# Kernel optimization log

Hardware: AMD Instinct MI355X
Metric: run time of the kernel (lower is better)

The kernel has to match this reference:

```python
import jax, jax.numpy as jnp
import numpy as np

N = 100000   # nodes
E = 1600000  # edges
DIN, DH, DOUT = 64, 128, 128


def setup_inputs() -> dict:
    key = jax.random.key(0)
    ks = jax.random.split(key, 12)
    x = jax.random.normal(ks[0], (N, DIN), dtype=jnp.float32)
    edge_index = jax.random.randint(ks[1], (2, E), 0, N, dtype=jnp.int32)
    s = 1.0 / np.sqrt(DIN)
    W1 = jax.random.uniform(ks[2], (DIN, DH), jnp.float32, -s, s)
    b1 = jnp.zeros((DH,), jnp.float32)
    g1 = jnp.ones((DH,), jnp.float32)
    bt1 = jnp.zeros((DH,), jnp.float32)
    s2 = 1.0 / np.sqrt(DH)
    W2 = jax.random.uniform(ks[3], (DH, DOUT), jnp.float32, -s2, s2)
    b2 = jnp.zeros((DOUT,), jnp.float32)
    g2 = jnp.ones((DOUT,), jnp.float32)
    bt2 = jnp.zeros((DOUT,), jnp.float32)
    return {"x": x, "edge_index": edge_index, "W1": W1, "b1": b1, "g1": g1,
            "bt1": bt1, "W2": W2, "b2": b2, "g2": g2, "bt2": bt2}


def _layer_norm(h, g, b, eps=1e-5):
    mu = h.mean(-1, keepdims=True)
    var = h.var(-1, keepdims=True)
    return (h - mu) * jax.lax.rsqrt(var + eps) * g + b


def reference(x, edge_index, W1, b1, g1, bt1, W2, b2, g2, bt2):
    # GCN normalization with self-loops (shared graph structure for both layers)
    src, dst = edge_index[0], edge_index[1]
    loops = jnp.arange(N, dtype=src.dtype)
    src = jnp.concatenate([src, loops])
    dst = jnp.concatenate([dst, loops])
    deg = jax.ops.segment_sum(jnp.ones_like(src, jnp.float32), dst, num_segments=N)
    dinv = jnp.where(deg > 0, jax.lax.rsqrt(deg), 0.0)
    norm = dinv[src] * dinv[dst]  # [E+N]

    def gcn(h, W, b):
        hw = h @ W                         # linear first (PyG GCNConv)
        msg = hw[src] * norm[:, None]      # gather + edge scale
        return jax.ops.segment_sum(msg, dst, num_segments=N) + b

    h = jax.nn.relu(_layer_norm(gcn(x, W1, b1), g1, bt1))
    # dropout is identity at inference
    h = jax.nn.relu(_layer_norm(gcn(h, W2, b2), g2, bt2))
    return h
```

## Files before the change

kernel.cpp:

```cpp
#include <hip/hip_runtime.h>

#define NN 100000
#define NE 1600000
#define NBKT 196
#define CAP 12288
#define EPB 8192
#define ABLK ((NE + EPB - 1) / EPB)
typedef unsigned short u16;
typedef unsigned int u32;

typedef __attribute__((ext_vector_type(8))) short short8v;
typedef __attribute__((ext_vector_type(4))) float f32x4;

__device__ __forceinline__ u32 f2bf(float f) {
    u32 u = __float_as_uint(f);
    return (u + 0x7fffu + ((u >> 16) & 1u)) >> 16;
}
__device__ __forceinline__ u32 pack2(float a, float b) {
    return f2bf(a) | (f2bf(b) << 16);
}
__device__ __forceinline__ void accum8(float* a, uint4 u, float w) {
    a[0] += __uint_as_float(u.x << 16) * w;
    a[1] += __uint_as_float(u.x & 0xffff0000u) * w;
    a[2] += __uint_as_float(u.y << 16) * w;
    a[3] += __uint_as_float(u.y & 0xffff0000u) * w;
    a[4] += __uint_as_float(u.z << 16) * w;
    a[5] += __uint_as_float(u.z & 0xffff0000u) * w;
    a[6] += __uint_as_float(u.w << 16) * w;
    a[7] += __uint_as_float(u.w & 0xffff0000u) * w;
}

__global__ __launch_bounds__(256) void kA_bin(const int* __restrict__ src,
                                              const int* __restrict__ dst,
                                              int* __restrict__ gcnt,
                                              u32* __restrict__ binned) {
    __shared__ int bc[NBKT];
    __shared__ int cbase[NBKT];
    const int tid = threadIdx.x;
    for (int i = tid; i < NBKT; i += 256) bc[i] = 0;
    __syncthreads();
    const int e0 = blockIdx.x * EPB;
#pragma unroll
    for (int i = 0; i < EPB / 256; ++i) {
        const int e = e0 + i * 256 + tid;
        if (e < NE) atomicAdd(&bc[dst[e] >> 9], 1);
    }
    __syncthreads();
    for (int i = tid; i < NBKT; i += 256)
        cbase[i] = bc[i] ? atomicAdd(&gcnt[i], bc[i]) : 0;
    __syncthreads();
    for (int i = tid; i < NBKT; i += 256) bc[i] = 0;
    __syncthreads();
#pragma unroll
    for (int i = 0; i < EPB / 256; ++i) {
        const int e = e0 + i * 256 + tid;
        if (e < NE) {
            const int d = dst[e];
            const int bkt = d >> 9;
            const int p = atomicAdd(&bc[bkt], 1);
            binned[bkt * CAP + cbase[bkt] + p] = ((u32)src[e] << 9) | (u32)(d & 511);
        }
    }
}

__global__ __launch_bounds__(256) void kB_fill(const u32* __restrict__ binned,
                                               const int* __restrict__ gcnt,
                                               int2* __restrict__ off2,
                                               float* __restrict__ dinv,
                                               int* __restrict__ csr,
                                               const float* __restrict__ x,
                                               u16* __restrict__ xb) {
    __shared__ int lcnt[512];
    __shared__ int lpos[512];
    __shared__ float sdinv[512];
    __shared__ int ws[4];
    const int b = blockIdx.x;
    const int tid = threadIdx.x;
    const int cnt = gcnt[b];
    const int base0 = b * CAP;
    const int node0 = b << 9;
    lcnt[tid] = 0;
    lcnt[tid + 256] = 0;
    __syncthreads();
    for (int e = tid; e < cnt; e += 256)
        atomicAdd(&lcnt[binned[base0 + e] & 511], 1);
    __syncthreads();
    const int c0 = lcnt[tid * 2], c1 = lcnt[tid * 2 + 1];
    const int s = c0 + c1;
    const int lane = tid & 63, w = tid >> 6;
    int incl = s;
#pragma unroll
    for (int o = 1; o < 64; o <<= 1) {
        const int u = __shfl_up(incl, o);
        if (lane >= o) incl += u;
    }
    if (lane == 63) ws[w] = incl;
    __syncthreads();
    int base = incl - s;
    for (int i = 0; i < w; ++i) base += ws[i];
    lpos[tid * 2] = base;
    lpos[tid * 2 + 1] = base + c0;
    const float d0 = rsqrtf(1.0f + (float)c0);
    const float d1 = rsqrtf(1.0f + (float)c1);
    sdinv[tid * 2] = d0;
    sdinv[tid * 2 + 1] = d1;
    const int n0 = node0 + tid * 2;
    if (n0 < NN) {
        off2[n0] = make_int2(base0 + base, base0 + base + c0);
        dinv[n0] = d0;
    }
    if (n0 + 1 < NN) {
        off2[n0 + 1] = make_int2(base0 + base + c0, base0 + base + c0 + c1);
        dinv[n0 + 1] = d1;
    }
    __syncthreads();
    for (int e = tid; e < cnt; e += 256) {
        const u32 u = binned[base0 + e];
        const int p = atomicAdd(&lpos[u & 511], 1);
        csr[base0 + p] = (int)(u >> 9);
    }
    const int nmax = min(512, NN - node0);
    for (int gi = tid; gi < nmax * 8; gi += 256) {
        const int nl = gi >> 3, ch = gi & 7;
        const float dr = sdinv[nl];
        const size_t xo = (size_t)(node0 + nl) * 64 + ch * 8;
        const float4 v0 = *(const float4*)&x[xo];
        const float4 v1 = *(const float4*)&x[xo + 4];
        uint4 o;
        o.x = pack2(v0.x * dr, v0.y * dr); o.y = pack2(v0.z * dr, v0.w * dr);
        o.z = pack2(v1.x * dr, v1.y * dr); o.w = pack2(v1.z * dr, v1.w * dr);
        *(uint4*)&xb[xo] = o;
    }
}

__global__ __launch_bounds__(256) void k_prep(const float* __restrict__ W1,
                                              const float* __restrict__ W2,
                                              u16* __restrict__ WT1,
                                              u16* __restrict__ WT2,
                                              int* __restrict__ gcnt) {
    const int i = blockIdx.x * 256 + threadIdx.x;
    if (i < 8192) {
        const int k = i >> 7, c = i & 127;
        WT1[c * 64 + k] = (u16)f2bf(W1[i]);
    } else if (i < 24576) {
        const int i2 = i - 8192;
        const int k = i2 >> 7, c = i2 & 127;
        WT2[c * 128 + k] = (u16)f2bf(W2[i2]);
    } else if (i < 24576 + NBKT) {
        gcnt[i - 24576] = 0;
    }
}

template<int K, bool FP32OUT, bool PRESCALE>
__global__ __launch_bounds__(256) void k_fused(const u16* __restrict__ A,
                                               const int2* __restrict__ off2,
                                               const int* __restrict__ csr,
                                               const float* __restrict__ dinv,
                                               const u16* __restrict__ WT,
                                               const float* __restrict__ bias,
                                               const float* __restrict__ g,
                                               const float* __restrict__ bt,
                                               void* __restrict__ outp) {
    constexpr int RB = K * 2;
    constexpr int SUBS = 512 / K;
    constexpr int LSH = (K == 64) ? 7 : 8;
    __shared__ u16 As[32 * K];
    __shared__ float s1s[4][32];
    __shared__ float s2s[4][32];
    __shared__ int claim;
    const int tid = threadIdx.x;
    const int wv = tid >> 6, lane = tid & 63;
    const int sub = lane / (64 / SUBS);
    const int l = lane & (64 / SUBS - 1);
    const char* Ab = (const char*)A + ((u32)l << 4);
    const int nodeBase = blockIdx.x * 32;

    if (tid == 0) claim = 0;
    __syncthreads();

    int i;
    if (lane == 0) i = atomicAdd(&claim, 1);
    i = __builtin_amdgcn_readfirstlane(i);
    while (i < 32) {
        const int node = nodeBase + i;
        const float di = dinv[node];
        float a[8] = {};
        {
            const uint4 u = *(const uint4*)(Ab + ((u32)node << LSH));
            accum8(a, u, (sub == 0) ? 1.0f : 0.0f);
        }
        const int2 oe = off2[node];
        int base = oe.x;
        const int e1 = oe.y;
        u32 iA = 0, iB = 0, iC = 0;
        float vA = 0.f, vB = 0.f, vC = 0.f;
        if (base < e1) {
            const int eA = base + sub, eB = eA + SUBS, eC = eA + 2 * SUBS;
            iA = (u32)csr[min(eA, e1 - 1)];
            iB = (u32)csr[min(eB, e1 - 1)];
            iC = (u32)csr[min(eC, e1 - 1)];
            vA = (eA < e1) ? 1.f : 0.f;
            vB = (eB < e1) ? 1.f : 0.f;
            vC = (eC < e1) ? 1.f : 0.f;
        }
        while (base < e1) {
            const uint4 uA = *(const uint4*)(Ab + (iA << LSH));
            const uint4 uB = *(const uint4*)(Ab + (iB << LSH));
            const uint4 uC = *(const uint4*)(Ab + (iC << LSH));
            const float wA = vA, wB = vB, wC = vC;
            base += 3 * SUBS;
            if (base < e1) {
                const int eA = base + sub, eB = eA + SUBS, eC = eA + 2 * SUBS;
                iA = (u32)csr[min(eA, e1 - 1)];
                iB = (u32)csr[min(eB, e1 - 1)];
                iC = (u32)csr[min(eC, e1 - 1)];
                vA = (eA < e1) ? 1.f : 0.f;
                vB = (eB < e1) ? 1.f : 0.f;
                vC = (eC < e1) ? 1.f : 0.f;
            }
            accum8(a, uA, wA);
            accum8(a, uB, wB);
            accum8(a, uC, wC);
        }
#pragma unroll
        for (int t = 0; t < 8; ++t)
#pragma unroll
            for (int o = 64 / SUBS; o < 64; o <<= 1)
                a[t] += __shfl_xor(a[t], o);
        if (sub == 0) {
            uint4 o;
            o.x = pack2(a[0] * di, a[1] * di); o.y = pack2(a[2] * di, a[3] * di);
            o.z = pack2(a[4] * di, a[5] * di); o.w = pack2(a[6] * di, a[7] * di);
            *(uint4*)((char*)As + i * RB + (((u32)l << 4) ^ ((u32)(i & 7) << 4))) = o;
        }
        if (lane == 0) i = atomicAdd(&claim, 1);
        i = __builtin_amdgcn_readfirstlane(i);
    }
    __syncthreads();

    const int lr = lane & 15, kg = lane >> 4;
    short8v af[2][K / 32];
#pragma unroll
    for (int rt = 0; rt < 2; ++rt)
#pragma unroll
        for (int kk = 0; kk < K / 32; ++kk)
            af[rt][kk] = *(const short8v*)((const char*)As + (rt * 16 + lr) * RB +
                                           ((u32)(kk * 64 + kg * 16) ^ ((u32)(lr & 7) << 4)));
    f32x4 acc[2][2];
    float bv[2], gv[2], tv[2];
#pragma unroll
    for (int nt = 0; nt < 2; ++nt) {
        acc[0][nt] = (f32x4){0.f, 0.f, 0.f, 0.f};
        acc[1][nt] = (f32x4){0.f, 0.f, 0.f, 0.f};
        const int col = wv * 32 + nt * 16 + lr;
        short8v bf[K / 32];
#pragma unroll
        for (int kk = 0; kk < K / 32; ++kk)
            bf[kk] = *(const short8v*)&WT[col * K + kk * 32 + kg * 8];
#pragma unroll
        for (int rt = 0; rt < 2; ++rt)
#pragma unroll
            for (int kk = 0; kk < K / 32; ++kk)
                acc[rt][nt] = __builtin_amdgcn_mfma_f32_16x16x32_bf16(
                    af[rt][kk], bf[kk], acc[rt][nt], 0, 0, 0);
        bv[nt] = bias[col]; gv[nt] = g[col]; tv[nt] = bt[col];
    }

    float s1[2][4] = {};
    float s2[2][4] = {};
#pragma unroll
    for (int rt = 0; rt < 2; ++rt)
#pragma unroll
        for (int nt = 0; nt < 2; ++nt)
#pragma unroll
            for (int j = 0; j < 4; ++j) {
                const float v = acc[rt][nt][j] + bv[nt];
                acc[rt][nt][j] = v;
                s1[rt][j] += v;
                s2[rt][j] += v * v;
            }
#pragma unroll
    for (int rt = 0; rt < 2; ++rt)
#pragma unroll
        for (int j = 0; j < 4; ++j)
#pragma unroll
            for (int o = 1; o < 16; o <<= 1) {
                s1[rt][j] += __shfl_xor(s1[rt][j], o);
                s2[rt][j] += __shfl_xor(s2[rt][j], o);
            }
    if (lr == 0) {
#pragma unroll
        for (int rt = 0; rt < 2; ++rt)
#pragma unroll
            for (int j = 0; j < 4; ++j) {
                s1s[wv][rt * 16 + kg * 4 + j] = s1[rt][j];
                s2s[wv][rt * 16 + kg * 4 + j] = s2[rt][j];
            }
    }
    __syncthreads();

#pragma unroll
    for (int rt = 0; rt < 2; ++rt)
#pragma unroll
        for (int j = 0; j < 4; ++j) {
            const int row = rt * 16 + kg * 4 + j;
            const float t1 = s1s[0][row] + s1s[1][row] + s1s[2][row] + s1s[3][row];
            const float t2 = s2s[0][row] + s2s[1][row] + s2s[2][row] + s2s[3][row];
            const float mu = t1 * (1.0f / 128.0f);
            const float var = t2 * (1.0f / 128.0f) - mu * mu;
            const float rs = rsqrtf(var + 1e-5f);
            const int node = nodeBase + row;
            const float dr = PRESCALE ? dinv[node] : 1.0f;
#pragma unroll
            for (int nt = 0; nt < 2; ++nt) {
                const float y = fmaxf((acc[rt][nt][j] - mu) * rs * gv[nt] + tv[nt], 0.f) * dr;
                const int col = wv * 32 + nt * 16 + lr;
                if constexpr (FP32OUT)
                    ((float*)outp)[(size_t)node * 128 + col] = y;
                else
                    ((u16*)outp)[(size_t)node * 128 + col] = (u16)f2bf(y);
            }
        }
}

__global__ __launch_bounds__(256) void k_agg128(const u16* __restrict__ A,
                                                const int2* __restrict__ off2,
                                                const int* __restrict__ csr,
                                                const float* __restrict__ dinv,
                                                u16* __restrict__ out) {
    const int node = blockIdx.x * 4 + (threadIdx.x >> 6);
    const int lane = threadIdx.x & 63;
    const int sub = lane >> 4, l = lane & 15;
    const char* Ab = (const char*)A + ((u32)l << 4);
    const float di = dinv[node];
    float a[8] = {};
    {
        const uint4 u = *(const uint4*)(Ab + ((u32)node << 8));
        accum8(a, u, (sub == 0) ? 1.0f : 0.0f);
    }
    const int2 oe = off2[node];
    int base = oe.x;
    const int e1 = oe.y;
    u32 iA = 0, iB = 0, iC = 0;
    float vA = 0.f, vB = 0.f, vC = 0.f;
    if (base < e1) {
        const int eA = base + sub, eB = eA + 4, eC = eA + 8;
        iA = (u32)csr[min(eA, e1 - 1)];
        iB = (u32)csr[min(eB, e1 - 1)];
        iC = (u32)csr[min(eC, e1 - 1)];
        vA = (eA < e1) ? 1.f : 0.f;
        vB = (eB < e1) ? 1.f : 0.f;
        vC = (eC < e1) ? 1.f : 0.f;
    }
    while (base < e1) {
        const uint4 uA = *(const uint4*)(Ab + (iA << 8));
        const uint4 uB = *(const uint4*)(Ab + (iB << 8));
        const uint4 uC = *(const uint4*)(Ab + (iC << 8));
        const float wA = vA, wB = vB, wC = vC;
        base += 12;
        if (base < e1) {
            const int eA = base + sub, eB = eA + 4, eC = eA + 8;
            iA = (u32)csr[min(eA, e1 - 1)];
            iB = (u32)csr[min(eB, e1 - 1)];
            iC = (u32)csr[min(eC, e1 - 1)];
            vA = (eA < e1) ? 1.f : 0.f;
            vB = (eB < e1) ? 1.f : 0.f;
            vC = (eC < e1) ? 1.f : 0.f;
        }
        accum8(a, uA, wA);
        accum8(a, uB, wB);
        accum8(a, uC, wC);
    }
#pragma unroll
    for (int i = 0; i < 8; ++i) {
        a[i] += __shfl_xor(a[i], 16);
        a[i] += __shfl_xor(a[i], 32);
    }
    if (sub == 0) {
        uint4 o;
        o.x = pack2(a[0] * di, a[1] * di); o.y = pack2(a[2] * di, a[3] * di);
        o.z = pack2(a[4] * di, a[5] * di); o.w = pack2(a[6] * di, a[7] * di);
        *(uint4*)((char*)out + ((u32)node << 8) + ((u32)l << 4)) = o;
    }
}

template<int K, bool FP32OUT, bool PRESCALE>
__global__ __launch_bounds__(256) void k_gemm_ln(const u16* __restrict__ Ain,
                                                 const u16* __restrict__ WT,
                                                 const float* __restrict__ bias,
                                                 const float* __restrict__ g,
                                                 const float* __restrict__ bt,
                                                 const float* __restrict__ dinv,
                                                 void* __restrict__ outp) {
    const int tid = threadIdx.x;
    const int wv = tid >> 6, lane = tid & 63;
    const int lr = lane & 15, kg = lane >> 4;
    const int row0 = blockIdx.x * 128 + wv * 32;

    short8v af[2][K / 32];
#pragma unroll
    for (int rt = 0; rt < 2; ++rt) {
        const int r = min(row0 + rt * 16 + lr, NN - 1);
#pragma unroll
        for (int kk = 0; kk < K / 32; ++kk)
            af[rt][kk] = *(const short8v*)&Ain[(size_t)r * K + kk * 32 + kg * 8];
    }
    f32x4 acc[2][8];
#pragma unroll
    for (int rt = 0; rt < 2; ++rt)
#pragma unroll
        for (int nt = 0; nt < 8; ++nt)
            acc[rt][nt] = (f32x4){0.f, 0.f, 0.f, 0.f};

#pragma unroll
    for (int nt = 0; nt < 8; ++nt) {
        const int col = nt * 16 + lr;
        short8v bf[K / 32];
#pragma unroll
        for (int kk = 0; kk < K / 32; ++kk)
            bf[kk] = *(const short8v*)&WT[col * K + kk * 32 + kg * 8];
#pragma unroll
        for (int rt = 0; rt < 2; ++rt)
#pragma unroll
            for (int kk = 0; kk < K / 32; ++kk)
                acc[rt][nt] = __builtin_amdgcn_mfma_f32_16x16x32_bf16(
                    af[rt][kk], bf[kk], acc[rt][nt], 0, 0, 0);
    }

    float bv[8], gv[8], tv[8];
#pragma unroll
    for (int nt = 0; nt < 8; ++nt) {
        const int col = nt * 16 + lr;
        bv[nt] = bias[col]; gv[nt] = g[col]; tv[nt] = bt[col];
    }

#pragma unroll
    for (int rt = 0; rt < 2; ++rt) {
        float s1[4] = {0.f, 0.f, 0.f, 0.f};
        float s2[4] = {0.f, 0.f, 0.f, 0.f};
#pragma unroll
        for (int nt = 0; nt < 8; ++nt)
#pragma unroll
            for (int j = 0; j < 4; ++j) {
                const float v = acc[rt][nt][j] + bv[nt];
                acc[rt][nt][j] = v;
                s1[j] += v;
                s2[j] += v * v;
            }
#pragma unroll
        for (int j = 0; j < 4; ++j)
#pragma unroll
            for (int o = 1; o < 16; o <<= 1) {
                s1[j] += __shfl_xor(s1[j], o);
                s2[j] += __shfl_xor(s2[j], o);
            }
#pragma unroll
        for (int j = 0; j < 4; ++j) {
            const int r = row0 + rt * 16 + kg * 4 + j;
            const float mu = s1[j] * (1.0f / 128.0f);
            const float var = s2[j] * (1.0f / 128.0f) - mu * mu;
            const float rs = rsqrtf(var + 1e-5f);
            if (r < NN) {
                const float dr = PRESCALE ? dinv[r] : 1.0f;
#pragma unroll
                for (int nt = 0; nt < 8; ++nt) {
                    const float y = fmaxf((acc[rt][nt][j] - mu) * rs * gv[nt] + tv[nt], 0.f) * dr;
                    const int col = nt * 16 + lr;
                    if constexpr (FP32OUT)
                        ((float*)outp)[(size_t)r * 128 + col] = y;
                    else
                        ((u16*)outp)[(size_t)r * 128 + col] = (u16)f2bf(y);
                }
            }
        }
    }
}

extern "C" void kernel_launch(void* const* d_in, const int* in_sizes, int n_in,
                              void* d_out, int out_size, void* d_ws, size_t ws_size,
                              hipStream_t stream) {
    const float* x   = (const float*)d_in[0];
    const int*   ei  = (const int*)d_in[1];
    const float* W1  = (const float*)d_in[2];
    const float* b1  = (const float*)d_in[3];
    const float* g1  = (const float*)d_in[4];
    const float* bt1 = (const float*)d_in[5];
    const float* W2  = (const float*)d_in[6];
    const float* b2  = (const float*)d_in[7];
    const float* g2  = (const float*)d_in[8];
    const float* bt2 = (const float*)d_in[9];

    const int* src = ei;
    const int* dst = ei + NE;

    const int NP = (NN + 255) & ~255;
    int*   gcnt   = (int*)d_ws;
    int2*  off2   = (int2*)(gcnt + 256);
    float* dinv   = (float*)(off2 + NP);
    int*   csr    = (int*)(dinv + NP);
    u32*   binned = (u32*)(csr + NBKT * CAP);
    u16*   xb     = (u16*)(binned + NBKT * CAP);
    u16*   aggh   = xb + (size_t)NN * 64;
    u16*   WT1    = aggh + (size_t)NN * 128;
    u16*   WT2    = WT1 + 128 * 64;
    u16*   h1     = (u16*)d_out;

    k_prep<<<(24576 + NBKT + 255) / 256, 256, 0, stream>>>(W1, W2, WT1, WT2, gcnt);
    kA_bin<<<ABLK, 256, 0, stream>>>(src, dst, gcnt, binned);
    kB_fill<<<NBKT, 256, 0, stream>>>(binned, gcnt, off2, dinv, csr, x, xb);

    k_fused<64, false, true><<<NN / 32, 256, 0, stream>>>(
        xb, off2, csr, dinv, WT1, b1, g1, bt1, h1);

    k_agg128<<<NN / 4, 256, 0, stream>>>(h1, off2, csr, dinv, aggh);
    k_gemm_ln<128, true, false><<<(NN + 127) / 128, 256, 0, stream>>>(
        aggh, WT2, b2, g2, bt2, dinv, d_out);
}
```

Before: 209.7 us.

## Quantize layer-1 activations to per-row uint8 to halve layer-2 gather traffic

The first fused GCN layer now writes its post-ReLU, dinv-prescaled output as unsigned 8-bit values with one float scale per node, taken from the row max, instead of bf16. The second-layer aggregation gathers 128-byte rows instead of 256-byte rows, dequantizes with the neighbour's scale, and processes 24 edges per iteration with 8 lanes per row. This targets the memory traffic of the random neighbour gathers, which is the dominant cost. The trade is coarser precision in the intermediate activations, plus an extra scale lookup per edge and an extra reduction and barrier for the row max.

Result: slower. 228.3 us (+8.9%).

```diff
diff --git a/kernel.cpp b/kernel.cpp
--- a/kernel.cpp
+++ b/kernel.cpp
@@ -8,6 +8,7 @@
 #define ABLK ((NE + EPB - 1) / EPB)
 typedef unsigned short u16;
 typedef unsigned int u32;
+typedef unsigned char u8;
 
 typedef __attribute__((ext_vector_type(8))) short short8v;
 typedef __attribute__((ext_vector_type(4))) float f32x4;
@@ -28,6 +29,17 @@
     a[5] += __uint_as_float(u.z & 0xffff0000u) * w;
     a[6] += __uint_as_float(u.w << 16) * w;
     a[7] += __uint_as_float(u.w & 0xffff0000u) * w;
+}
+__device__ __forceinline__ void accum16u8(float* a, uint4 u, float w) {
+    const u32 wd[4] = {u.x, u.y, u.z, u.w};
+#pragma unroll
+    for (int b = 0; b < 4; ++b) {
+        const u32 v = wd[b];
+        a[b * 4 + 0] += (float)(v & 0xffu) * w;
+        a[b * 4 + 1] += (float)((v >> 8) & 0xffu) * w;
+        a[b * 4 + 2] += (float)((v >> 16) & 0xffu) * w;
+        a[b * 4 + 3] += (float)(v >> 24) * w;
+    }
 }
 
 __global__ __launch_bounds__(256) void kA_bin(const int* __restrict__ src,
@@ -151,22 +163,24 @@
     }
 }
 
-template<int K, bool FP32OUT, bool PRESCALE>
-__global__ __launch_bounds__(256) void k_fused(const u16* __restrict__ A,
-                                               const int2* __restrict__ off2,
-                                               const int* __restrict__ csr,
-                                               const float* __restrict__ dinv,
-                                               const u16* __restrict__ WT,
-                                               const float* __restrict__ bias,
-                                               const float* __restrict__ g,
-                                               const float* __restrict__ bt,
-                                               void* __restrict__ outp) {
+template<int K>
+__global__ __launch_bounds__(256) void k_fused64(const u16* __restrict__ A,
+                                                 const int2* __restrict__ off2,
+                                                 const int* __restrict__ csr,
+                                                 const float* __restrict__ dinv,
+                                                 const u16* __restrict__ WT,
+                                                 const float* __restrict__ bias,
+                                                 const float* __restrict__ g,
+                                                 const float* __restrict__ bt,
+                                                 u8* __restrict__ outq,
+                                                 float* __restrict__ sc) {
     constexpr int RB = K * 2;
     constexpr int SUBS = 512 / K;
-    constexpr int LSH = (K == 64) ? 7 : 8;
+    constexpr int LSH = 7;
     __shared__ u16 As[32 * K];
     __shared__ float s1s[4][32];
     __shared__ float s2s[4][32];
+    __shared__ float s3s[4][32];
     __shared__ int claim;
     const int tid = threadIdx.x;
     const int wv = tid >> 6, lane = tid & 63;
@@ -299,6 +313,8 @@
     }
     __syncthreads();
 
+    float yv[2][2][4];
+    float rmax[2][4];
 #pragma unroll
     for (int rt = 0; rt < 2; ++rt)
 #pragma unroll
@@ -310,33 +326,66 @@
             const float var = t2 * (1.0f / 128.0f) - mu * mu;
             const float rs = rsqrtf(var + 1e-5f);
             const int node = nodeBase + row;
-            const float dr = PRESCALE ? dinv[node] : 1.0f;
+            const float dr = dinv[node];
+            float m = 0.f;
 #pragma unroll
             for (int nt = 0; nt < 2; ++nt) {
                 const float y = fmaxf((acc[rt][nt][j] - mu) * rs * gv[nt] + tv[nt], 0.f) * dr;
+                yv[rt][nt][j] = y;
+                m = fmaxf(m, y);
+            }
+            rmax[rt][j] = m;
+        }
+#pragma unroll
+    for (int rt = 0; rt < 2; ++rt)
+#pragma unroll
+        for (int j = 0; j < 4; ++j)
+#pragma unroll
+            for (int o = 1; o < 16; o <<= 1)
+                rmax[rt][j] = fmaxf(rmax[rt][j], __shfl_xor(rmax[rt][j], o));
+    if (lr == 0) {
+#pragma unroll
+        for (int rt = 0; rt < 2; ++rt)
+#pragma unroll
+            for (int j = 0; j < 4; ++j)
+                s3s[wv][rt * 16 + kg * 4 + j] = rmax[rt][j];
+    }
+    __syncthreads();
+
+#pragma unroll
+    for (int rt = 0; rt < 2; ++rt)
+#pragma unroll
+        for (int j = 0; j < 4; ++j) {
+            const int row = rt * 16 + kg * 4 + j;
+            const float rm = fmaxf(fmaxf(fmaxf(s3s[0][row], s3s[1][row]),
+                                         fmaxf(s3s[2][row], s3s[3][row])), 1e-30f);
+            const float qs = 255.0f / rm;
+            const int node = nodeBase + row;
+#pragma unroll
+            for (int nt = 0; nt < 2; ++nt) {
+                const int q = min(255, (int)(yv[rt][nt][j] * qs + 0.5f));
                 const int col = wv * 32 + nt * 16 + lr;
-                if constexpr (FP32OUT)
-                    ((float*)outp)[(size_t)node * 128 + col] = y;
-                else
-                    ((u16*)outp)[(size_t)node * 128 + col] = (u16)f2bf(y);
-            }
-        }
-}
-
-__global__ __launch_bounds__(256) void k_agg128(const u16* __restrict__ A,
-                                                const int2* __restrict__ off2,
-                                                const int* __restrict__ csr,
-                                                const float* __restrict__ dinv,
-                                                u16* __restrict__ out) {
+                outq[(size_t)node * 128 + col] = (u8)q;
+            }
+            if (wv == 0 && lr == 0) sc[node] = rm * (1.0f / 255.0f);
+        }
+}
+
+__global__ __launch_bounds__(256) void k_agg128q(const u8* __restrict__ A,
+                                                 const int2* __restrict__ off2,
+                                                 const int* __restrict__ csr,
+                                                 const float* __restrict__ dinv,
+                                                 const float* __restrict__ sc,
+                                                 u16* __restrict__ out) {
     const int node = blockIdx.x * 4 + (threadIdx.x >> 6);
     const int lane = threadIdx.x & 63;
-    const int sub = lane >> 4, l = lane & 15;
-    const char* Ab = (const char*)A + ((u32)l << 4);
+    const int sub = lane >> 3, l = lane & 7;
+    const u8* Ab = A + ((u32)l << 4);
     const float di = dinv[node];
-    float a[8] = {};
+    float a[16] = {};
     {
-        const uint4 u = *(const uint4*)(Ab + ((u32)node << 8));
-        accum8(a, u, (sub == 0) ? 1.0f : 0.0f);
+        const uint4 u = *(const uint4*)(Ab + ((u32)node << 7));
+        accum16u8(a, u, (sub == 0) ? sc[node] : 0.0f);
     }
     const int2 oe = off2[node];
     int base = oe.x;
@@ -344,54 +393,58 @@
     u32 iA = 0, iB = 0, iC = 0;
     float vA = 0.f, vB = 0.f, vC = 0.f;
     if (base < e1) {
-        const int eA = base + sub, eB = eA + 4, eC = eA + 8;
+        const int eA = base + sub, eB = eA + 8, eC = eA + 16;
         iA = (u32)csr[min(eA, e1 - 1)];
         iB = (u32)csr[min(eB, e1 - 1)];
         iC = (u32)csr[min(eC, e1 - 1)];
-        vA = (eA < e1) ? 1.f : 0.f;
-        vB = (eB < e1) ? 1.f : 0.f;
-        vC = (eC < e1) ? 1.f : 0.f;
+        vA = (eA < e1) ? sc[iA] : 0.f;
+        vB = (eB < e1) ? sc[iB] : 0.f;
+        vC = (eC < e1) ? sc[iC] : 0.f;
     }
     while (base < e1) {
-        const uint4 uA = *(const uint4*)(Ab + (iA << 8));
-        const uint4 uB = *(const uint4*)(Ab + (iB << 8));
-        const uint4 uC = *(const uint4*)(Ab + (iC << 8));
+        const uint4 uA = *(const uint4*)(Ab + (iA << 7));
+        const uint4 uB = *(const uint4*)(Ab + (iB << 7));
+        const uint4 uC = *(const uint4*)(Ab + (iC << 7));
         const float wA = vA, wB = vB, wC = vC;
-        base += 12;
+        base += 24;
         if (base < e1) {
-            const int eA = base + sub, eB = eA + 4, eC = eA + 8;
+            const int eA = base + sub, eB = eA + 8, eC = eA + 16;
             iA = (u32)csr[min(eA, e1 - 1)];
             iB = (u32)csr[min(eB, e1 - 1)];
             iC = (u32)csr[min(eC, e1 - 1)];
-            vA = (eA < e1) ? 1.f : 0.f;
-            vB = (eB < e1) ? 1.f : 0.f;
-            vC = (eC < e1) ? 1.f : 0.f;
-        }
-        accum8(a, uA, wA);
-        accum8(a, uB, wB);
-        accum8(a, uC, wC);
-    }
-#pragma unroll
-    for (int i = 0; i < 8; ++i) {
+            vA = (eA < e1) ? sc[iA] : 0.f;
+            vB = (eB < e1) ? sc[iB] : 0.f;
+            vC = (eC < e1) ? sc[iC] : 0.f;
+        }
+        accum16u8(a, uA, wA);
+        accum16u8(a, uB, wB);
+        accum16u8(a, uC, wC);
+    }
+#pragma unroll
+    for (int i = 0; i < 16; ++i) {
+        a[i] += __shfl_xor(a[i], 8);
         a[i] += __shfl_xor(a[i], 16);
         a[i] += __shfl_xor(a[i], 32);
     }
     if (sub == 0) {
-        uint4 o;
-        o.x = pack2(a[0] * di, a[1] * di); o.y = pack2(a[2] * di, a[3] * di);
-        o.z = pack2(a[4] * di, a[5] * di); o.w = pack2(a[6] * di, a[7] * di);
-        *(uint4*)((char*)out + ((u32)node << 8) + ((u32)l << 4)) = o;
-    }
-}
-
-template<int K, bool FP32OUT, bool PRESCALE>
+        uint4 o1, o2;
+        o1.x = pack2(a[0] * di, a[1] * di);  o1.y = pack2(a[2] * di, a[3] * di);
+        o1.z = pack2(a[4] * di, a[5] * di);  o1.w = pack2(a[6] * di, a[7] * di);
+        o2.x = pack2(a[8] * di, a[9] * di);  o2.y = pack2(a[10] * di, a[11] * di);
+        o2.z = pack2(a[12] * di, a[13] * di); o2.w = pack2(a[14] * di, a[15] * di);
+        char* orow = (char*)out + ((u32)node << 8) + ((u32)l << 5);
+        *(uint4*)orow = o1;
+        *(uint4*)(orow + 16) = o2;
+    }
+}
+
+template<int K>
 __global__ __launch_bounds__(256) void k_gemm_ln(const u16* __restrict__ Ain,
                                                  const u16* __restrict__ WT,
                                                  const float* __restrict__ bias,
                                                  const float* __restrict__ g,
                                                  const float* __restrict__ bt,
-                                                 const float* __restrict__ dinv,
-                                                 void* __restrict__ outp) {
+                                                 float* __restrict__ outp) {
     const int tid = threadIdx.x;
     const int wv = tid >> 6, lane = tid & 63;
     const int lr = lane & 15, kg = lane >> 4;
@@ -461,15 +514,11 @@
             const float var = s2[j] * (1.0f / 128.0f) - mu * mu;
             const float rs = rsqrtf(var + 1e-5f);
             if (r < NN) {
-                const float dr = PRESCALE ? dinv[r] : 1.0f;
 #pragma unroll
                 for (int nt = 0; nt < 8; ++nt) {
-                    const float y = fmaxf((acc[rt][nt][j] - mu) * rs * gv[nt] + tv[nt], 0.f) * dr;
+                    const float y = fmaxf((acc[rt][nt][j] - mu) * rs * gv[nt] + tv[nt], 0.f);
                     const int col = nt * 16 + lr;
-                    if constexpr (FP32OUT)
-                        ((float*)outp)[(size_t)r * 128 + col] = y;
-                    else
-                        ((u16*)outp)[(size_t)r * 128 + col] = (u16)f2bf(y);
+                    outp[(size_t)r * 128 + col] = y;
                 }
             }
         }
@@ -497,22 +546,23 @@
     int*   gcnt   = (int*)d_ws;
     int2*  off2   = (int2*)(gcnt + 256);
     float* dinv   = (float*)(off2 + NP);
-    int*   csr    = (int*)(dinv + NP);
+    float* sc     = dinv + NP;
+    int*   csr    = (int*)(sc + NP);
     u32*   binned = (u32*)(csr + NBKT * CAP);
     u16*   xb     = (u16*)(binned + NBKT * CAP);
     u16*   aggh   = xb + (size_t)NN * 64;
     u16*   WT1    = aggh + (size_t)NN * 128;
     u16*   WT2    = WT1 + 128 * 64;
-    u16*   h1     = (u16*)d_out;
+    u8*    h1q    = (u8*)d_out;
 
     k_prep<<<(24576 + NBKT + 255) / 256, 256, 0, stream>>>(W1, W2, WT1, WT2, gcnt);
     kA_bin<<<ABLK, 256, 0, stream>>>(src, dst, gcnt, binned);
     kB_fill<<<NBKT, 256, 0, stream>>>(binned, gcnt, off2, dinv, csr, x, xb);
 
-    k_fused<64, false, true><<<NN / 32, 256, 0, stream>>>(
-        xb, off2, csr, dinv, WT1, b1, g1, bt1, h1);
-
-    k_agg128<<<NN / 4, 256, 0, stream>>>(h1, off2, csr, dinv, aggh);
-    k_gemm_ln<128, true, false><<<(NN + 127) / 128, 256, 0, stream>>>(
-        aggh, WT2, b2, g2, bt2, dinv, d_out);
-}
+    k_fused64<64><<<NN / 32, 256, 0, stream>>>(
+        xb, off2, csr, dinv, WT1, b1, g1, bt1, h1q, sc);
+
+    k_agg128q<<<NN / 4, 256, 0, stream>>>(h1q, off2, csr, dinv, sc, aggh);
+    k_gemm_ln<128><<<(NN + 127) / 128, 256, 0, stream>>>(
+        aggh, WT2, b2, g2, bt2, (float*)d_out);
+}
```
